# Kernel optimization log

Measured on AMD Instinct MI355X. Metric: run time of the kernel, lower is better.

Reference implementation:

```python
import jax, jax.numpy as jnp
import numpy as np

DIST_IND = 7.0   # disturbance_indicator
SLOPE_MIN = 0.0
SLOPE_MAX = 2.0


def setup_inputs() -> dict:
    key = jax.random.key(0)
    k1, k2 = jax.random.split(key)
    B, Y, H, W = 16, 32, 256, 256
    out = jax.random.normal(k1, (B, Y, H, W), dtype=jnp.float32)
    target = jax.random.normal(k2, (B, Y, H, W), dtype=jnp.float32)
    return {"out": out, "target": target}


def _regress(n, sx, sxx, sy, sxy):
    # least-squares slope/intercept from sufficient statistics; window invalid if n <= 2
    valid = n >= 3.0
    n_safe = jnp.maximum(n, 1.0)
    cov = sxy - sx * sy / n_safe
    var = sxx - sx * sx / n_safe
    var_safe = jnp.where(var > 0, var, 1.0)
    slope = jnp.clip(cov / var_safe, SLOPE_MIN, SLOPE_MAX)
    intercept = (sy - slope * sx) / n_safe
    return slope, intercept, valid


def reference(out, target):
    # target is unused (precalculation_function=None), kept for signature fidelity
    B, Y, H, W = out.shape
    dt = out.dtype
    t = jnp.arange(Y, dtype=dt)

    # ---- disturbance index (torch.no_grad block) ----
    diff = jnp.diff(out, axis=1)
    diff = jnp.concatenate([jnp.full((B, 1, H, W), -DIST_IND, dt), diff], axis=1)
    # full_disturbance_window = False -> zero diff at t=1 and t=Y-1
    diff = diff.at[:, 1].set(0.0).at[:, -1].set(0.0)
    idx = jnp.argmin(jax.lax.stop_gradient(diff), axis=1)  # [B,H,W] int

    # ---- per-window-start sufficient statistics (O(T) per output via einsum) ----
    f = jnp.arange(Y, dtype=dt)[:, None]          # window start f: [Y,1]
    mb = (t[None, :] < f).astype(dt)              # prefix mask  out[:, :f]
    ma = (t[None, :] >= f).astype(dt)             # suffix mask  out[:, f:]
    xb = t[None, :] * mb
    xa = (t[None, :] - f) * ma

    sy_b = jnp.einsum('ft,bthw->fbhw', mb, out)
    sxy_b = jnp.einsum('ft,bthw->fbhw', xb, out)
    sy_a = jnp.einsum('ft,bthw->fbhw', ma, out)
    sxy_a = jnp.einsum('ft,bthw->fbhw', xa, out)

    n_b, sx_b, sxx_b = mb.sum(1), xb.sum(1), (xb * t).sum(1)                    # [Y]
    n_a, sx_a, sxx_a = ma.sum(1), xa.sum(1), (xa * (t[None, :] - f)).sum(1)     # [Y]

    # select stats at f = disturbance_idx per pixel
    idx4 = idx[None]  # [1,B,H,W]
    gather = lambda a: jnp.take_along_axis(a, idx4, axis=0)[0]

    slope_b, int_b, val_b = _regress(n_b[idx], sx_b[idx], sxx_b[idx], gather(sy_b), gather(sxy_b))
    slope_a, int_a, val_a = _regress(n_a[idx], sx_a[idx], sxx_a[idx], gather(sy_a), gather(sxy_a))

    tt = t[None, :, None, None]                   # [1,Y,1,1]
    idxe = idx[:, None].astype(dt)                # [B,1,H,W]
    pred_b = jax.lax.stop_gradient(slope_b[:, None] * tt + int_b[:, None])
    pred_a = jax.lax.stop_gradient(slope_a[:, None] * (tt - idxe) + int_a[:, None])
    mask_b = (tt < idxe).astype(dt)
    mask_a = 1.0 - mask_b
    res_b = (mask_b * (out - pred_b) ** 2).sum(axis=1)  # [B,H,W]
    res_a = (mask_a * (out - pred_a) ** 2).sum(axis=1)

    loss = (jnp.where(val_b, res_b, 0.0) + jnp.where(val_a, res_a, 0.0)) / Y
    return loss.mean()
```

## Files before the change

kernel.cpp:

```cpp
#include <hip/hip_runtime.h>

#define Bn 16
#define Yn 32
#define Hn 256
#define Wn 256
#define HWn (Hn * Wn)
#define NPIX (Bn * HWn)
#define DIST_IND_F 7.0f

#define OUT_SCALE (1.0f / ((float)Yn * (float)NPIX))

__device__ __forceinline__ void regress_f(float n, float sx, float sxx,
                                          float sy, float sxy,
                                          float& slope, float& inter, bool& valid) {
    valid = (n >= 3.0f);
    float n_safe = fmaxf(n, 1.0f);
    float cov = sxy - sx * sy / n_safe;
    float var = sxx - sx * sx / n_safe;
    float var_safe = (var > 0.0f) ? var : 1.0f;
    float s = cov / var_safe;
    s = fminf(fmaxf(s, 0.0f), 2.0f);
    slope = s;
    inter = (sy - s * sx) / n_safe;
}

__device__ __forceinline__ float pixel_loss(const float* v) {
    float dmin = -DIST_IND_F;
    int idx = 0;
#pragma unroll
    for (int y = 2; y < Yn - 1; ++y) {
        float d = v[y] - v[y - 1];
        if (d < dmin) { dmin = d; idx = y; }
    }

    float sy_b = 0.0f, sxy_b = 0.0f, sy_a = 0.0f, sxy_a = 0.0f;
#pragma unroll
    for (int t = 0; t < Yn; ++t) {
        bool bef = (t < idx);
        float xb = (float)t;
        float xa = (float)(t - idx);
        if (bef) { sy_b += v[t]; sxy_b += xb * v[t]; }
        else     { sy_a += v[t]; sxy_a += xa * v[t]; }
    }

    const int nb = idx;
    const int na = Yn - idx;
    const float sx_b  = (float)((nb * (nb - 1)) / 2);
    const float sxx_b = (float)(((nb - 1) * nb * (2 * nb - 1)) / 6);
    const float sx_a  = (float)((na * (na - 1)) / 2);
    const float sxx_a = (float)(((na - 1) * na * (2 * na - 1)) / 6);

    float slope_b, int_b, slope_a, int_a;
    bool val_b, val_a;
    regress_f((float)nb, sx_b, sxx_b, sy_b, sxy_b, slope_b, int_b, val_b);
    regress_f((float)na, sx_a, sxx_a, sy_a, sxy_a, slope_a, int_a, val_a);

    float res_b = 0.0f, res_a = 0.0f;
#pragma unroll
    for (int t = 0; t < Yn; ++t) {
        float pb = slope_b * (float)t + int_b;
        float pa = slope_a * (float)(t - idx) + int_a;
        float rb = v[t] - pb;
        float ra = v[t] - pa;
        if (t < idx) res_b += rb * rb;
        else         res_a += ra * ra;
    }

    return (val_b ? res_b : 0.0f) + (val_a ? res_a : 0.0f);
}

__global__ __launch_bounds__(256)
void DisturbanceRegressionLoss_kernel(const float* __restrict__ out,
                                      float* __restrict__ loss_out) {
    const int g = blockIdx.x * 256 + threadIdx.x;
    const int b = g >> 14;
    const int hw4 = g & ((HWn / 4) - 1);
    const float4* base = (const float4*)(out + (size_t)b * (Yn * HWn)) + hw4;

    float4 v4[Yn];
#pragma unroll
    for (int y = 0; y < Yn; ++y) v4[y] = base[(size_t)y * (HWn / 4)];

    float loss = 0.0f;
#pragma unroll
    for (int c = 0; c < 4; ++c) {
        float v[Yn];
#pragma unroll
        for (int y = 0; y < Yn; ++y) {
            v[y] = (c == 0) ? v4[y].x : (c == 1) ? v4[y].y : (c == 2) ? v4[y].z : v4[y].w;
        }
        loss += pixel_loss(v);
    }

#pragma unroll
    for (int off = 32; off > 0; off >>= 1)
        loss += __shfl_down(loss, off, 64);

    __shared__ float smem[4];
    const int lane = threadIdx.x & 63;
    const int wid  = threadIdx.x >> 6;
    if (lane == 0) smem[wid] = loss;
    __syncthreads();
    if (threadIdx.x == 0) {
        float s = smem[0] + smem[1] + smem[2] + smem[3];
        atomicAdd(loss_out, s * OUT_SCALE);
    }
}

extern "C" void kernel_launch(void* const* d_in, const int* in_sizes, int n_in,
                              void* d_out, int out_size, void* d_ws, size_t ws_size,
                              hipStream_t stream) {
    const float* out_in = (const float*)d_in[0];
    float* loss = (float*)d_out;

    hipMemsetAsync(loss, 0, sizeof(float) * (size_t)out_size, stream);

    dim3 grid(NPIX / 4 / 256), block(256);
    DisturbanceRegressionLoss_kernel<<<grid, block, 0, stream>>>(out_in, loss);
}
```

Measured before the change: 247.1 us.

## Compute residuals from running sufficient statistics in a single streaming pass

The per-pixel work becomes one streaming pass that keeps running sums of v, t*v and v*v, and snapshots the prefix sums whenever a new argmin is found. The suffix sums are then derived by subtraction, and the squared residuals come from a closed-form expansion, so the three loops over 32 timesteps and the 32-entry float4 register array are gone. Loads are double-buffered in chunks of 8 timesteps, and the launch bounds now request 4 blocks per SM. The aim is lower register pressure, higher occupancy and fewer ALU ops, at the cost of float cancellation error in the expanded residual formula.

```diff
diff --git a/kernel.cpp b/kernel.cpp
--- a/kernel.cpp
+++ b/kernel.cpp
@@ -24,72 +24,95 @@
     inter = (sy - s * sx) / n_safe;
 }
 
-__device__ __forceinline__ float pixel_loss(const float* v) {
-    float dmin = -DIST_IND_F;
-    int idx = 0;
-#pragma unroll
-    for (int y = 2; y < Yn - 1; ++y) {
-        float d = v[y] - v[y - 1];
-        if (d < dmin) { dmin = d; idx = y; }
-    }
-
-    float sy_b = 0.0f, sxy_b = 0.0f, sy_a = 0.0f, sxy_a = 0.0f;
-#pragma unroll
-    for (int t = 0; t < Yn; ++t) {
-        bool bef = (t < idx);
-        float xb = (float)t;
-        float xa = (float)(t - idx);
-        if (bef) { sy_b += v[t]; sxy_b += xb * v[t]; }
-        else     { sy_a += v[t]; sxy_a += xa * v[t]; }
-    }
-
-    const int nb = idx;
-    const int na = Yn - idx;
-    const float sx_b  = (float)((nb * (nb - 1)) / 2);
-    const float sxx_b = (float)(((nb - 1) * nb * (2 * nb - 1)) / 6);
-    const float sx_a  = (float)((na * (na - 1)) / 2);
-    const float sxx_a = (float)(((na - 1) * na * (2 * na - 1)) / 6);
-
-    float slope_b, int_b, slope_a, int_a;
-    bool val_b, val_a;
-    regress_f((float)nb, sx_b, sxx_b, sy_b, sxy_b, slope_b, int_b, val_b);
-    regress_f((float)na, sx_a, sxx_a, sy_a, sxy_a, slope_a, int_a, val_a);
-
-    float res_b = 0.0f, res_a = 0.0f;
-#pragma unroll
-    for (int t = 0; t < Yn; ++t) {
-        float pb = slope_b * (float)t + int_b;
-        float pa = slope_a * (float)(t - idx) + int_a;
-        float rb = v[t] - pb;
-        float ra = v[t] - pa;
-        if (t < idx) res_b += rb * rb;
-        else         res_a += ra * ra;
-    }
-
-    return (val_b ? res_b : 0.0f) + (val_a ? res_a : 0.0f);
-}
-
-__global__ __launch_bounds__(256)
+__global__ __launch_bounds__(256, 4)
 void DisturbanceRegressionLoss_kernel(const float* __restrict__ out,
                                       float* __restrict__ loss_out) {
     const int g = blockIdx.x * 256 + threadIdx.x;
     const int b = g >> 14;
     const int hw4 = g & ((HWn / 4) - 1);
     const float4* base = (const float4*)(out + (size_t)b * (Yn * HWn)) + hw4;
+    const size_t stride = HWn / 4;
 
-    float4 v4[Yn];
+    float vprev[4], dmin[4], s1[4], sx1[4], svv[4], s1b[4], sxb[4], svvb[4];
+    int idx[4];
 #pragma unroll
-    for (int y = 0; y < Yn; ++y) v4[y] = base[(size_t)y * (HWn / 4)];
+    for (int c = 0; c < 4; ++c) {
+        vprev[c] = 0.0f; dmin[c] = -DIST_IND_F;
+        s1[c] = 0.0f; sx1[c] = 0.0f; svv[c] = 0.0f;
+        s1b[c] = 0.0f; sxb[c] = 0.0f; svvb[c] = 0.0f;
+        idx[c] = 0;
+    }
+
+    float4 buf[2][8];
+#pragma unroll
+    for (int j = 0; j < 8; ++j) buf[0][j] = base[(size_t)j * stride];
+
+#pragma unroll
+    for (int k = 0; k < 4; ++k) {
+        if (k < 3) {
+#pragma unroll
+            for (int j = 0; j < 8; ++j)
+                buf[(k + 1) & 1][j] = base[(size_t)((k + 1) * 8 + j) * stride];
+        }
+#pragma unroll
+        for (int j = 0; j < 8; ++j) {
+            const int t = k * 8 + j;
+            const float tf = (float)t;
+            float4 vv = buf[k & 1][j];
+            float vc[4] = {vv.x, vv.y, vv.z, vv.w};
+#pragma unroll
+            for (int c = 0; c < 4; ++c) {
+                float v = vc[c];
+                if (t >= 2 && t <= 30) {
+                    float d = v - vprev[c];
+                    if (d < dmin[c]) {
+                        dmin[c] = d; idx[c] = t;
+                        s1b[c] = s1[c];
+                        sxb[c] = sx1[c];
+                        svvb[c] = svv[c];
+                    }
+                }
+                s1[c] += v;
+                sx1[c] = fmaf(tf, v, sx1[c]);
+                svv[c] = fmaf(v, v, svv[c]);
+                vprev[c] = v;
+            }
+        }
+    }
 
     float loss = 0.0f;
 #pragma unroll
     for (int c = 0; c < 4; ++c) {
-        float v[Yn];
-#pragma unroll
-        for (int y = 0; y < Yn; ++y) {
-            v[y] = (c == 0) ? v4[y].x : (c == 1) ? v4[y].y : (c == 2) ? v4[y].z : v4[y].w;
-        }
-        loss += pixel_loss(v);
+        const int nb = idx[c];
+        const int na = Yn - nb;
+        const float fnb = (float)nb, fna = (float)na;
+        const float sx_b  = (float)((nb * (nb - 1)) / 2);
+        const float sxx_b = (float)(((nb - 1) * nb * (2 * nb - 1)) / 6);
+        const float sx_a  = (float)((na * (na - 1)) / 2);
+        const float sxx_a = (float)(((na - 1) * na * (2 * na - 1)) / 6);
+
+        const float sy_b  = s1b[c];
+        const float sxy_b = sxb[c];
+        const float svv_b = svvb[c];
+        const float sy_a  = s1[c] - sy_b;
+        const float sxy_a = (sx1[c] - sxb[c]) - fnb * sy_a;
+        const float svv_a = svv[c] - svv_b;
+
+        float slope_b, int_b, slope_a, int_a;
+        bool val_b, val_a;
+        regress_f(fnb, sx_b, sxx_b, sy_b, sxy_b, slope_b, int_b, val_b);
+        regress_f(fna, sx_a, sxx_a, sy_a, sxy_a, slope_a, int_a, val_a);
+
+        float res_b = svv_b - 2.0f * slope_b * sxy_b - 2.0f * int_b * sy_b
+                    + slope_b * slope_b * sxx_b
+                    + 2.0f * slope_b * int_b * sx_b
+                    + int_b * int_b * fnb;
+        float res_a = svv_a - 2.0f * slope_a * sxy_a - 2.0f * int_a * sy_a
+                    + slope_a * slope_a * sxx_a
+                    + 2.0f * slope_a * int_a * sx_a
+                    + int_a * int_a * fna;
+
+        loss += (val_b ? res_b : 0.0f) + (val_a ? res_a : 0.0f);
     }
 
 #pragma unroll
```

After: 244.5 us. No clear change (-1.1%).
